# Optimization experiments

Hardware: AMD Instinct MI355X
Metric: run time of the kernel (lower is better)

## Reference

```python
import jax, jax.numpy as jnp
import numpy as np

EPS = 1e-7
LAMBDA_RANK = 0.5
NEG = -1e30  # finite stand-in for -inf (keeps logsumexp grads finite)

B = 8192
N_BINS = 4


def setup_inputs() -> dict:
    key = jax.random.key(0)
    k1, k2, k3, k4 = jax.random.split(key, 4)
    outputs = jax.random.normal(k1, (B, N_BINS), dtype=jnp.float32)
    t = jax.random.uniform(k2, (B,), dtype=jnp.float32) * 100.0  # survival times
    y = jax.random.randint(k3, (B,), 0, N_BINS, dtype=jnp.int32)  # interval index
    c = jax.random.randint(k4, (B,), 0, 2, dtype=jnp.int32)       # 0=event, 1=censored
    return {"outputs": outputs, "t": t, "y": y, "c": c}


def reference(outputs, t, y, c):
    dt = outputs.dtype
    # ---- NLL survival loss ----
    hazards = jax.nn.sigmoid(outputs)                       # [B, K]
    S = jnp.cumprod(1.0 - hazards, axis=1)                  # [B, K]
    S_pad = jnp.concatenate([jnp.ones((outputs.shape[0], 1), dt), S], axis=1)  # [B, K+1]
    yv = y[:, None].astype(jnp.int32)
    s_prev = jnp.clip(jnp.take_along_axis(S_pad, yv, axis=1), EPS)
    h_this = jnp.clip(jnp.take_along_axis(hazards, yv, axis=1), EPS)
    s_this = jnp.clip(jnp.take_along_axis(S_pad, yv + 1, axis=1), EPS)
    cf = c[:, None].astype(dt)
    uncensored = -(1.0 - cf) * (jnp.log(s_prev) + jnp.log(h_this))
    censored = -cf * jnp.log(s_this)
    loss_nll = (censored + uncensored).mean()  # alpha == 0, reduction == 'mean'

    # ---- pairwise rank loss (vectorized over all i) ----
    risk = -jnp.sum(S, axis=1)                               # [B]
    event = (c == 0)                                         # [B] bool
    pair_mask = t[None, :] > t[:, None]                      # [B, B]; (i, j): t_j > t_i
    masked = jnp.where(pair_mask, risk[None, :], NEG)        # [B, B]
    lse = jax.nn.logsumexp(masked, axis=1)                   # [B]
    valid = event & jnp.any(pair_mask, axis=1)               # rows contributing
    contrib = jnp.where(valid, lse - risk, jnp.zeros((), dt))
    count = jnp.sum(valid.astype(dt))
    loss_rank = jnp.where(count > 0, contrib.sum() / jnp.maximum(count, 1.0), jnp.zeros((), dt))

    return loss_nll + LAMBDA_RANK * loss_rank
```

## Files before the change

### kernel.cpp

```cpp
#include <hip/hip_runtime.h>

#define BROWS 8192
#define EPSF 1e-7f
#define NBLK 256
#define RPB 32
#define TPB 1024

__device__ __forceinline__ float wave_reduce_sum(float v) {
    #pragma unroll
    for (int off = 32; off > 0; off >>= 1) v += __shfl_xor(v, off, 64);
    return v;
}

__device__ __forceinline__ float rcp_fast(float x) {
    return __builtin_amdgcn_rcpf(x);
}

__global__ __launch_bounds__(TPB, 4) void fused_kernel(
        const float4* __restrict__ outputs, const float* __restrict__ t,
        const int* __restrict__ y, const int* __restrict__ c,
        float4* __restrict__ part) {
    __shared__ float2 te[BROWS];
    int tid = threadIdx.x, lane = tid & 63, wave = tid >> 6;
    int rowbase = blockIdx.x * RPB;

    #pragma unroll
    for (int u = 0; u < BROWS / TPB; ++u) {
        int j = tid + u * TPB;
        float4 o = outputs[j];
        float q0 = rcp_fast(1.f + __expf(o.x));
        float q1 = rcp_fast(1.f + __expf(o.y));
        float q2 = rcp_fast(1.f + __expf(o.z));
        float q3 = rcp_fast(1.f + __expf(o.w));
        float S1 = q0, S2 = S1 * q1, S3 = S2 * q2, S4 = S3 * q3;
        float risk = -(S1 + S2 + S3 + S4);
        te[j] = make_float2(t[j], __expf(risk));
    }
    __syncthreads();

    float t0 = te[rowbase + 2 * wave].x;
    float t1 = te[rowbase + 2 * wave + 1].x;
    float a0 = 0.f, a1 = 0.f;
    #pragma unroll 8
    for (int k = lane; k < BROWS; k += 64) {
        float2 p = te[k];
        a0 += (p.x > t0) ? p.y : 0.f;
        a1 += (p.x > t1) ? p.y : 0.f;
    }
    a0 = wave_reduce_sum(a0);
    a1 = wave_reduce_sum(a1);
    __syncthreads();

    float* wsum = (float*)te;
    if (lane == 0) { wsum[2 * wave] = a0; wsum[2 * wave + 1] = a1; }
    __syncthreads();

    if (wave == 0) {
        float contrib = 0.f, cnt = 0.f, nll = 0.f;
        if (lane < RPB) {
            int row = rowbase + lane;
            float s = wsum[lane];
            float4 o = outputs[row];
            float q0 = rcp_fast(1.f + __expf(o.x));
            float q1 = rcp_fast(1.f + __expf(o.y));
            float q2 = rcp_fast(1.f + __expf(o.z));
            float q3 = rcp_fast(1.f + __expf(o.w));
            float S1 = q0, S2 = S1 * q1, S3 = S2 * q2, S4 = S3 * q3;
            float risk = -(S1 + S2 + S3 + S4);
            int yi = y[row], ci = c[row];
            float s_prev = (yi == 0) ? 1.f : (yi == 1) ? S1 : (yi == 2) ? S2 : S3;
            float s_this = (yi == 0) ? S1  : (yi == 1) ? S2 : (yi == 2) ? S3 : S4;
            float xsel   = (yi == 0) ? o.x : (yi == 1) ? o.y : (yi == 2) ? o.z : o.w;
            float h_this = rcp_fast(1.f + __expf(-xsel));
            float cf = (float)ci;
            nll = -cf * __logf(fmaxf(s_this, EPSF))
                  - (1.f - cf) * (__logf(fmaxf(s_prev, EPSF)) + __logf(fmaxf(h_this, EPSF)));
            bool valid = (ci == 0) && (s > 0.f);
            contrib = valid ? (__logf(s) - risk) : 0.f;
            cnt     = valid ? 1.f : 0.f;
        }
        contrib = wave_reduce_sum(contrib);
        cnt     = wave_reduce_sum(cnt);
        nll     = wave_reduce_sum(nll);
        if (lane == 0) part[blockIdx.x] = make_float4(contrib, cnt, nll, 0.f);
    }
}

__global__ __launch_bounds__(NBLK) void combine_kernel(
        const float4* __restrict__ part, float* __restrict__ out) {
    __shared__ float sh[12];
    int tid = threadIdx.x, lane = tid & 63, wave = tid >> 6;
    float4 p = part[tid];
    float rs = wave_reduce_sum(p.x);
    float cs = wave_reduce_sum(p.y);
    float ns = wave_reduce_sum(p.z);
    if (lane == 0) { sh[wave] = rs; sh[4 + wave] = cs; sh[8 + wave] = ns; }
    __syncthreads();
    if (tid == 0) {
        float b = sh[0] + sh[1] + sh[2] + sh[3];
        float d = sh[4] + sh[5] + sh[6] + sh[7];
        float a = sh[8] + sh[9] + sh[10] + sh[11];
        float loss_nll  = a / (float)BROWS;
        float loss_rank = (d > 0.f) ? (b / fmaxf(d, 1.f)) : 0.f;
        out[0] = loss_nll + 0.5f * loss_rank;
    }
}

extern "C" void kernel_launch(void* const* d_in, const int* in_sizes, int n_in,
                              void* d_out, int out_size, void* d_ws, size_t ws_size,
                              hipStream_t stream) {
    const float4* outputs = (const float4*)d_in[0];
    const float*  t       = (const float*)d_in[1];
    const int*    y       = (const int*)d_in[2];
    const int*    c       = (const int*)d_in[3];
    float* out = (float*)d_out;
    float4* part = (float4*)d_ws;

    fused_kernel<<<NBLK, TPB, 0, stream>>>(outputs, t, y, c, part);
    combine_kernel<<<1, NBLK, 0, stream>>>(part, out);
}
```

Baseline: 16.41 us.

## Fold combine kernel into fused kernel via spin-wait on per-block flags

```diff
diff --git a/kernel.cpp b/kernel.cpp
--- a/kernel.cpp
+++ b/kernel.cpp
@@ -11,18 +11,23 @@
     for (int off = 32; off > 0; off >>= 1) v += __shfl_xor(v, off, 64);
     return v;
 }
+__device__ __forceinline__ float rcp_fast(float x) { return __builtin_amdgcn_rcpf(x); }
 
-__device__ __forceinline__ float rcp_fast(float x) {
-    return __builtin_amdgcn_rcpf(x);
+__device__ __forceinline__ float aload(const float* p) {
+    return __hip_atomic_load(p, __ATOMIC_RELAXED, __HIP_MEMORY_SCOPE_AGENT);
+}
+__device__ __forceinline__ void astore(float* p, float v) {
+    __hip_atomic_store(p, v, __ATOMIC_RELAXED, __HIP_MEMORY_SCOPE_AGENT);
 }
 
 __global__ __launch_bounds__(TPB, 4) void fused_kernel(
         const float4* __restrict__ outputs, const float* __restrict__ t,
         const int* __restrict__ y, const int* __restrict__ c,
-        float4* __restrict__ part) {
+        float* __restrict__ part, float* __restrict__ out) {
     __shared__ float2 te[BROWS];
     int tid = threadIdx.x, lane = tid & 63, wave = tid >> 6;
-    int rowbase = blockIdx.x * RPB;
+    int b = blockIdx.x;
+    int rowbase = b * RPB;
 
     #pragma unroll
     for (int u = 0; u < BROWS / TPB; ++u) {
@@ -41,11 +46,14 @@
     float t0 = te[rowbase + 2 * wave].x;
     float t1 = te[rowbase + 2 * wave + 1].x;
     float a0 = 0.f, a1 = 0.f;
+    const float4* te4 = (const float4*)te;
     #pragma unroll 8
-    for (int k = lane; k < BROWS; k += 64) {
-        float2 p = te[k];
-        a0 += (p.x > t0) ? p.y : 0.f;
-        a1 += (p.x > t1) ? p.y : 0.f;
+    for (int k = lane; k < BROWS / 2; k += 64) {
+        float4 q = te4[k];
+        a0 += (q.x > t0) ? q.y : 0.f;
+        a1 += (q.x > t1) ? q.y : 0.f;
+        a0 += (q.z > t0) ? q.w : 0.f;
+        a1 += (q.z > t1) ? q.w : 0.f;
     }
     a0 = wave_reduce_sum(a0);
     a1 = wave_reduce_sum(a1);
@@ -82,27 +90,42 @@
         contrib = wave_reduce_sum(contrib);
         cnt     = wave_reduce_sum(cnt);
         nll     = wave_reduce_sum(nll);
-        if (lane == 0) part[blockIdx.x] = make_float4(contrib, cnt, nll, 0.f);
+        if (lane == 0) {
+            astore(&part[b * 4 + 0], contrib);
+            astore(&part[b * 4 + 1], cnt);
+            astore(&part[b * 4 + 2], nll);
+            asm volatile("s_waitcnt vmcnt(0)" ::: "memory");
+            astore(&part[b * 4 + 3], 1.0f);
+        }
     }
-}
 
-__global__ __launch_bounds__(NBLK) void combine_kernel(
-        const float4* __restrict__ part, float* __restrict__ out) {
-    __shared__ float sh[12];
-    int tid = threadIdx.x, lane = tid & 63, wave = tid >> 6;
-    float4 p = part[tid];
-    float rs = wave_reduce_sum(p.x);
-    float cs = wave_reduce_sum(p.y);
-    float ns = wave_reduce_sum(p.z);
-    if (lane == 0) { sh[wave] = rs; sh[4 + wave] = cs; sh[8 + wave] = ns; }
-    __syncthreads();
-    if (tid == 0) {
-        float b = sh[0] + sh[1] + sh[2] + sh[3];
-        float d = sh[4] + sh[5] + sh[6] + sh[7];
-        float a = sh[8] + sh[9] + sh[10] + sh[11];
-        float loss_nll  = a / (float)BROWS;
-        float loss_rank = (d > 0.f) ? (b / fmaxf(d, 1.f)) : 0.f;
-        out[0] = loss_nll + 0.5f * loss_rank;
+    if (b == 0 && wave == 0) {
+        int p0 = lane * 4;
+        for (int sweep = 0; sweep < (1 << 17); ++sweep) {
+            int ok = 1;
+            #pragma unroll
+            for (int k = 0; k < 4; ++k)
+                ok &= (aload(&part[(p0 + k) * 4 + 3]) == 1.0f);
+            if (__all(ok)) break;
+            __builtin_amdgcn_s_sleep(8);
+        }
+        asm volatile("" ::: "memory");
+        float rs = 0.f, cs = 0.f, ns = 0.f;
+        #pragma unroll
+        for (int k = 0; k < 4; ++k) {
+            int pb = (p0 + k) * 4;
+            rs += aload(&part[pb + 0]);
+            cs += aload(&part[pb + 1]);
+            ns += aload(&part[pb + 2]);
+        }
+        rs = wave_reduce_sum(rs);
+        cs = wave_reduce_sum(cs);
+        ns = wave_reduce_sum(ns);
+        if (lane == 0) {
+            float loss_nll  = ns / (float)BROWS;
+            float loss_rank = (cs > 0.f) ? (rs / fmaxf(cs, 1.f)) : 0.f;
+            out[0] = loss_nll + 0.5f * loss_rank;
+        }
     }
 }
 
@@ -113,9 +136,8 @@
     const float*  t       = (const float*)d_in[1];
     const int*    y       = (const int*)d_in[2];
     const int*    c       = (const int*)d_in[3];
-    float* out = (float*)d_out;
-    float4* part = (float4*)d_ws;
+    float* out  = (float*)d_out;
+    float* part = (float*)d_ws;
 
-    fused_kernel<<<NBLK, TPB, 0, stream>>>(outputs, t, y, c, part);
-    combine_kernel<<<1, NBLK, 0, stream>>>(part, out);
+    fused_kernel<<<NBLK, TPB, 0, stream>>>(outputs, t, y, c, part, out);
 }
```

After: 16.56 us. About the same (+0.9%).
